# Optimization experiments

Hardware: AMD Instinct MI355X
Metric: run time of the kernel (lower is better)

The kernel has to match this reference:

```python
import jax, jax.numpy as jnp
import numpy as np

N_NODES = 100000
N_EDGES = 50000
NNZ = 800000
D_IN = 128
D_OUT = 128


def setup_inputs() -> dict:
    key = jax.random.key(0)
    k1, k2, k3, k4, k5 = jax.random.split(key, 5)
    x_0 = jax.random.normal(k1, (N_NODES, D_IN), dtype=jnp.float32)
    W = jax.random.normal(k2, (D_OUT, D_IN), dtype=jnp.float32) / np.sqrt(D_IN)
    b = jax.random.normal(k3, (D_OUT,), dtype=jnp.float32) * 0.01
    node_ids = jax.random.randint(k4, (NNZ,), 0, N_NODES, dtype=jnp.int32)
    edge_ids = jax.random.randint(k5, (NNZ,), 0, N_EDGES, dtype=jnp.int32)
    return {"x_0": x_0, "W": W, "b": b, "node_ids": node_ids, "edge_ids": edge_ids}


def reference(x_0, W, b, node_ids, edge_ids):
    # Linear transform (no batchnorm: use_bn=False)
    x = x_0 @ W.T + b  # [n_nodes, out_channels]

    # Step 1: hyperedge aggregation (e_aggr='sum'):  m_{0->1} = B_1^T x, reduce=sum
    m01 = jax.ops.segment_sum(x[node_ids], edge_ids, num_segments=N_EDGES)  # [n_edges, d]

    # Step 2: node aggregation (v_aggr='mean'):  m_{1->0} = B_1 m_{0->1}, reduce=mean
    s = jax.ops.segment_sum(m01[edge_ids], node_ids, num_segments=N_NODES)  # [n_nodes, d]
    cnt = jax.ops.segment_sum(jnp.ones((NNZ,), dtype=x.dtype), node_ids, num_segments=N_NODES)
    m10 = s / jnp.maximum(cnt, 1.0)[:, None]

    # Step 3: SAGE update (residual add)
    return x + m10
```

## Files before the change

kernel.cpp:

```cpp
#include <hip/hip_runtime.h>
#include <hip/hip_bf16.h>

#define NN 100000
#define NE 50000
#define NZ 800000
#define D  128
#define NSEG (NE + NN)
#define FILL_P 4
#define FILL_B 782
#define G_GEMM 782
#define G_HIST 391

typedef __bf16 bf16x8 __attribute__((ext_vector_type(8)));
typedef float f32x4 __attribute__((ext_vector_type(4)));

static __device__ __forceinline__ unsigned short f2bf(float f) {
  union { float f; unsigned u; } v; v.f = f;
  unsigned r = (v.u + 0x7FFFu + ((v.u >> 16) & 1u)) >> 16;
  return (unsigned short)r;
}
static __device__ __forceinline__ float bf2f(unsigned short h) {
  union { unsigned u; float f; } v; v.u = ((unsigned)h) << 16;
  return v.f;
}

__global__ __launch_bounds__(256) void unisage_gemm_hist(const float* __restrict__ x0,
                                                         const float* __restrict__ W,
                                                         const float* __restrict__ bias,
                                                         unsigned short* __restrict__ xb,
                                                         const int* __restrict__ nid,
                                                         const int* __restrict__ eid,
                                                         int* __restrict__ cnt,
                                                         unsigned short* __restrict__ rank_e,
                                                         unsigned short* __restrict__ rank_n) {
  __shared__ __bf16 Wl[128][136];
  if (blockIdx.x < G_HIST) {
    int base = (blockIdx.x * 256 + threadIdx.x) * 8;
    if (base >= NZ) return;
    int4 ea = *(const int4*)(eid + base);
    int4 eb = *(const int4*)(eid + base + 4);
    int4 na = *(const int4*)(nid + base);
    int4 nb = *(const int4*)(nid + base + 4);
    int e[8] = {ea.x, ea.y, ea.z, ea.w, eb.x, eb.y, eb.z, eb.w};
    int v[8] = {na.x, na.y, na.z, na.w, nb.x, nb.y, nb.z, nb.w};
    unsigned short re[8], rn[8];
#pragma unroll
    for (int j = 0; j < 8; ++j) re[j] = (unsigned short)atomicAdd(&cnt[e[j]], 1);
#pragma unroll
    for (int j = 0; j < 8; ++j) rn[j] = (unsigned short)atomicAdd(&cnt[NE + v[j]], 1);
    ushort4 r0 = {re[0], re[1], re[2], re[3]};
    ushort4 r1 = {re[4], re[5], re[6], re[7]};
    ushort4 s0 = {rn[0], rn[1], rn[2], rn[3]};
    ushort4 s1 = {rn[4], rn[5], rn[6], rn[7]};
    *(ushort4*)(rank_e + base) = r0;
    *(ushort4*)(rank_e + base + 4) = r1;
    *(ushort4*)(rank_n + base) = s0;
    *(ushort4*)(rank_n + base + 4) = s1;
  } else {
    const int t = threadIdx.x;
#pragma unroll
    for (int i = 0; i < 16; ++i) {
      int idx = i * 1024 + t * 4;
      int dout = idx >> 7;
      int k = idx & 127;
      float4 wv = *(const float4*)(W + idx);
      Wl[dout][k + 0] = (__bf16)wv.x;
      Wl[dout][k + 1] = (__bf16)wv.y;
      Wl[dout][k + 2] = (__bf16)wv.z;
      Wl[dout][k + 3] = (__bf16)wv.w;
    }
    __syncthreads();

    const int wave = t >> 6;
    const int lane = t & 63;
    const int lr = lane & 15;
    const int lg = lane >> 4;
    const int rowbase = (blockIdx.x - G_HIST) * 128 + wave * 32;

    f32x4 acc[2][8] = {};

#pragma unroll
    for (int ks = 0; ks < 4; ++ks) {
      const int k0 = ks * 32 + lg * 8;
      bf16x8 wf[8];
#pragma unroll
      for (int cf = 0; cf < 8; ++cf)
        wf[cf] = *(const bf16x8*)&Wl[cf * 16 + lr][k0];
#pragma unroll
      for (int rf = 0; rf < 2; ++rf) {
        int row = rowbase + rf * 16 + lr;
        row = row < NN ? row : NN - 1;
        const float* src = x0 + (size_t)row * D + k0;
        float4 f0 = *(const float4*)(src);
        float4 f1 = *(const float4*)(src + 4);
        bf16x8 xf;
        xf[0] = (__bf16)f0.x; xf[1] = (__bf16)f0.y;
        xf[2] = (__bf16)f0.z; xf[3] = (__bf16)f0.w;
        xf[4] = (__bf16)f1.x; xf[5] = (__bf16)f1.y;
        xf[6] = (__bf16)f1.z; xf[7] = (__bf16)f1.w;
#pragma unroll
        for (int cf = 0; cf < 8; ++cf)
          acc[rf][cf] = __builtin_amdgcn_mfma_f32_16x16x32_bf16(wf[cf], xf, acc[rf][cf], 0, 0, 0);
      }
    }

#pragma unroll
    for (int cf = 0; cf < 8; ++cf) {
      float4 bv = *(const float4*)(bias + cf * 16 + lg * 4);
#pragma unroll
      for (int rf = 0; rf < 2; ++rf) {
        int row = rowbase + rf * 16 + lr;
        if (row < NN) {
          ushort4 o;
          o.x = f2bf(acc[rf][cf][0] + bv.x);
          o.y = f2bf(acc[rf][cf][1] + bv.y);
          o.z = f2bf(acc[rf][cf][2] + bv.z);
          o.w = f2bf(acc[rf][cf][3] + bv.w);
          *(ushort4*)(xb + (size_t)row * D + cf * 16 + lg * 4) = o;
        }
      }
    }
  }
}

__global__ void unisage_scan_k1(const int* __restrict__ in, int* __restrict__ bsum, int n) {
  __shared__ int sh[256];
  int t = threadIdx.x;
  int base = blockIdx.x * 1024 + t * 4;
  int s = 0;
#pragma unroll
  for (int j = 0; j < 4; ++j)
    if (base + j < n) s += in[base + j];
  sh[t] = s;
  __syncthreads();
  for (int o = 128; o > 0; o >>= 1) {
    if (t < o) sh[t] += sh[t + o];
    __syncthreads();
  }
  if (t == 0) bsum[blockIdx.x] = sh[0];
}

__global__ void unisage_scan_k3(const int* __restrict__ in, const int* __restrict__ bsum,
                                int* __restrict__ out, int n, int nb) {
  __shared__ int sh[256];
  int t = threadIdx.x;
  int bv = (t < nb) ? bsum[t] : 0;
  sh[t] = bv;
  __syncthreads();
  for (int o = 1; o < 256; o <<= 1) {
    int add = (t >= o) ? sh[t - o] : 0;
    __syncthreads();
    sh[t] += add;
    __syncthreads();
  }
  int bbase = (blockIdx.x == 0) ? 0 : sh[blockIdx.x - 1];
  __syncthreads();

  int base = blockIdx.x * 1024 + t * 4;
  int v[4];
#pragma unroll
  for (int j = 0; j < 4; ++j) v[j] = (base + j < n) ? in[base + j] : 0;
  int tsum = v[0] + v[1] + v[2] + v[3];
  sh[t] = tsum;
  __syncthreads();
  for (int o = 1; o < 256; o <<= 1) {
    int add = (t >= o) ? sh[t - o] : 0;
    __syncthreads();
    sh[t] += add;
    __syncthreads();
  }
  int run = sh[t] - tsum + bbase;
#pragma unroll
  for (int j = 0; j < 4; ++j) {
    if (base + j < n) out[base + j] = run;
    run += v[j];
  }
}

__global__ void unisage_fill(const int* __restrict__ nid, const int* __restrict__ eid,
                             const unsigned short* __restrict__ rank_e,
                             const unsigned short* __restrict__ rank_n,
                             const int* __restrict__ off,
                             int* __restrict__ csr_e, int* __restrict__ csr_n) {
  const int R = (NSEG + FILL_P - 1) / FILL_P;
  int pass = blockIdx.x / FILL_B;
  int base = ((blockIdx.x % FILL_B) * 256 + threadIdx.x) * 4;
  if (base >= NZ) return;
  int lo = pass * R, hi = lo + R;
  int4 e4 = *(const int4*)(eid + base);
  int4 n4 = *(const int4*)(nid + base);
  ushort4 re4 = *(const ushort4*)(rank_e + base);
  ushort4 rn4 = *(const ushort4*)(rank_n + base);
  int e[4] = {e4.x, e4.y, e4.z, e4.w};
  int v[4] = {n4.x, n4.y, n4.z, n4.w};
  unsigned short re[4] = {re4.x, re4.y, re4.z, re4.w};
  unsigned short rn[4] = {rn4.x, rn4.y, rn4.z, rn4.w};
#pragma unroll
  for (int j = 0; j < 4; ++j) {
    if (e[j] >= lo && e[j] < hi) csr_e[off[e[j]] + (int)re[j]] = v[j];
    int s = NE + v[j];
    if (s >= lo && s < hi) csr_n[off[s] + (int)rn[j] - NZ] = e[j];
  }
}

#define QRED(x) { x += __shfl_xor(x, 16, 64); x += __shfl_xor(x, 32, 64); }

__global__ void unisage_edge_agg(const unsigned short* __restrict__ xb,
                                 const int* __restrict__ csr_e,
                                 const int* __restrict__ off, const int* __restrict__ cnt,
                                 unsigned short* __restrict__ m01b) {
  int w = (blockIdx.x * 256 + threadIdx.x) >> 6;
  int lane = threadIdx.x & 63;
  if (w >= NE) return;
  int quad = lane >> 4;
  int sl = lane & 15;
  int beg = off[w];
  int deg = cnt[w];
  int end = beg + deg;
  float a0 = 0, a1 = 0, a2 = 0, a3 = 0, a4 = 0, a5 = 0, a6 = 0, a7 = 0;
  for (int base = beg; base < end; base += 64) {
    int m = min(64, end - base);
    int idx = (lane < m) ? csr_e[base + lane] : 0;
    int iters = (m + 3) >> 2;
    for (int jj = 0; jj < iters; ++jj) {
      int p = 4 * jj + quad;
      int r = __shfl(idx, p, 64);
      if (p < m) {
        uint4 vv = *(const uint4*)(xb + (size_t)r * D + sl * 8);
        a0 += bf2f((unsigned short)(vv.x & 0xffffu)); a1 += bf2f((unsigned short)(vv.x >> 16));
        a2 += bf2f((unsigned short)(vv.y & 0xffffu)); a3 += bf2f((unsigned short)(vv.y >> 16));
        a4 += bf2f((unsigned short)(vv.z & 0xffffu)); a5 += bf2f((unsigned short)(vv.z >> 16));
        a6 += bf2f((unsigned short)(vv.w & 0xffffu)); a7 += bf2f((unsigned short)(vv.w >> 16));
      }
    }
  }
  QRED(a0) QRED(a1) QRED(a2) QRED(a3) QRED(a4) QRED(a5) QRED(a6) QRED(a7)
  if (quad == 0) {
    uint4 o;
    o.x = (unsigned)f2bf(a0) | ((unsigned)f2bf(a1) << 16);
    o.y = (unsigned)f2bf(a2) | ((unsigned)f2bf(a3) << 16);
    o.z = (unsigned)f2bf(a4) | ((unsigned)f2bf(a5) << 16);
    o.w = (unsigned)f2bf(a6) | ((unsigned)f2bf(a7) << 16);
    *(uint4*)(m01b + (size_t)w * D + sl * 8) = o;
  }
}

__global__ void unisage_node_agg(const unsigned short* __restrict__ xb,
                                 const unsigned short* __restrict__ m01b,
                                 const int* __restrict__ csr_n,
                                 const int* __restrict__ off, const int* __restrict__ cnt,
                                 float* __restrict__ out) {
  int wv = (blockIdx.x * 256 + threadIdx.x) >> 6;
  int lane = threadIdx.x & 63;
  int half = lane >> 5;
  int sub = lane & 31;
  int rg = sub >> 4;
  int sl = sub & 15;
  int w = wv * 2 + half;
  if (w >= NN) return;
  int deg = cnt[NE + w];
  int beg = off[NE + w] - NZ;
  int end = beg + deg;
  float a0 = 0, a1 = 0, a2 = 0, a3 = 0, a4 = 0, a5 = 0, a6 = 0, a7 = 0;
  for (int base = beg; base < end; base += 32) {
    int m = min(32, end - base);
    int idx = (sub < m) ? csr_n[base + sub] : 0;
    int iters = (m + 1) >> 1;
    for (int jj = 0; jj < iters; ++jj) {
      int p = 2 * jj + rg;
      int r = __shfl(idx, half * 32 + p, 64);
      if (p < m) {
        uint4 vv = *(const uint4*)(m01b + (size_t)r * D + sl * 8);
        a0 += bf2f((unsigned short)(vv.x & 0xffffu)); a1 += bf2f((unsigned short)(vv.x >> 16));
        a2 += bf2f((unsigned short)(vv.y & 0xffffu)); a3 += bf2f((unsigned short)(vv.y >> 16));
        a4 += bf2f((unsigned short)(vv.z & 0xffffu)); a5 += bf2f((unsigned short)(vv.z >> 16));
        a6 += bf2f((unsigned short)(vv.w & 0xffffu)); a7 += bf2f((unsigned short)(vv.w >> 16));
      }
    }
  }
  a0 += __shfl_xor(a0, 16, 64); a1 += __shfl_xor(a1, 16, 64);
  a2 += __shfl_xor(a2, 16, 64); a3 += __shfl_xor(a3, 16, 64);
  a4 += __shfl_xor(a4, 16, 64); a5 += __shfl_xor(a5, 16, 64);
  a6 += __shfl_xor(a6, 16, 64); a7 += __shfl_xor(a7, 16, 64);
  if (rg == 0) {
    float inv = 1.0f / fmaxf((float)deg, 1.0f);
    uint4 xr = *(const uint4*)(xb + (size_t)w * D + sl * 8);
    f32x4 o0, o1;
    o0[0] = bf2f((unsigned short)(xr.x & 0xffffu)) + a0 * inv;
    o0[1] = bf2f((unsigned short)(xr.x >> 16))     + a1 * inv;
    o0[2] = bf2f((unsigned short)(xr.y & 0xffffu)) + a2 * inv;
    o0[3] = bf2f((unsigned short)(xr.y >> 16))     + a3 * inv;
    o1[0] = bf2f((unsigned short)(xr.z & 0xffffu)) + a4 * inv;
    o1[1] = bf2f((unsigned short)(xr.z >> 16))     + a5 * inv;
    o1[2] = bf2f((unsigned short)(xr.w & 0xffffu)) + a6 * inv;
    o1[3] = bf2f((unsigned short)(xr.w >> 16))     + a7 * inv;
    __builtin_nontemporal_store(o0, (f32x4*)(out + (size_t)w * D + sl * 8));
    __builtin_nontemporal_store(o1, (f32x4*)(out + (size_t)w * D + sl * 8 + 4));
  }
}

extern "C" void kernel_launch(void* const* d_in, const int* in_sizes, int n_in,
                              void* d_out, int out_size, void* d_ws, size_t ws_size,
                              hipStream_t stream) {
  const float* x0   = (const float*)d_in[0];
  const float* W    = (const float*)d_in[1];
  const float* bias = (const float*)d_in[2];
  const int* nid    = (const int*)d_in[3];
  const int* eid    = (const int*)d_in[4];
  float* out = (float*)d_out;

  unsigned short* xb   = (unsigned short*)d_ws;
  unsigned short* m01b = xb + (size_t)NN * D;
  int* cnt   = (int*)(m01b + (size_t)NE * D);
  int* off   = cnt + 150016;
  unsigned short* rank_e = (unsigned short*)(off + 150016);
  unsigned short* rank_n = rank_e + NZ;
  int* csr_e = (int*)(rank_n + NZ);
  int* csr_n = csr_e + NZ;
  int* bsum  = csr_n + NZ;

  hipMemsetAsync(cnt, 0, NSEG * sizeof(int), stream);

  unisage_gemm_hist<<<G_HIST + G_GEMM, 256, 0, stream>>>(x0, W, bias, xb, nid, eid,
                                                         cnt, rank_e, rank_n);

  const int nb = (NSEG + 1023) / 1024;
  unisage_scan_k1<<<nb, 256, 0, stream>>>(cnt, bsum, NSEG);
  unisage_scan_k3<<<nb, 256, 0, stream>>>(cnt, bsum, off, NSEG, nb);

  unisage_fill<<<FILL_P * FILL_B, 256, 0, stream>>>(nid, eid, rank_e, rank_n, off, csr_e, csr_n);

  unisage_edge_agg<<<(NE * 64) / 256, 256, 0, stream>>>(xb, csr_e, off, cnt, m01b);
  unisage_node_agg<<<(NN / 2 * 64) / 256, 256, 0, stream>>>(xb, m01b, csr_n, off, cnt, out);
}
```

Baseline: 191.0 us.

## Split CSR fill and overlap node-side fill with edge aggregation

The combined fill kernel is split in two. The edge-CSR fill now runs alone in 2 passes over the edge range. The node-CSR fill, also 2 passes, is merged into the edge aggregation kernel as extra blocks, so those scatter writes run alongside the gather-sum instead of before it. This is meant to hide the node-side fill latency and drop its serialization. In exchange, the two block types in the merged launch now compete for bandwidth, and the edge fill is no longer split into the finer passes of the old 4-pass scheme.

New measurement: 189.0 us. No clear change (-1.1%).

```diff
diff --git a/kernel.cpp b/kernel.cpp
--- a/kernel.cpp
+++ b/kernel.cpp
@@ -6,10 +6,11 @@
 #define NZ 800000
 #define D  128
 #define NSEG (NE + NN)
-#define FILL_P 4
 #define FILL_B 782
 #define G_GEMM 782
 #define G_HIST 391
+#define G_EDGE 12500
+#define G_FILLN (2 * FILL_B)
 
 typedef __bf16 bf16x8 __attribute__((ext_vector_type(8)));
 typedef float f32x4 __attribute__((ext_vector_type(4)));
@@ -177,12 +178,11 @@
   }
 }
 
-__global__ void unisage_fill(const int* __restrict__ nid, const int* __restrict__ eid,
-                             const unsigned short* __restrict__ rank_e,
-                             const unsigned short* __restrict__ rank_n,
-                             const int* __restrict__ off,
-                             int* __restrict__ csr_e, int* __restrict__ csr_n) {
-  const int R = (NSEG + FILL_P - 1) / FILL_P;
+__global__ void unisage_fill_e(const int* __restrict__ nid, const int* __restrict__ eid,
+                               const unsigned short* __restrict__ rank_e,
+                               const int* __restrict__ off,
+                               int* __restrict__ csr_e) {
+  const int R = NE / 2;
   int pass = blockIdx.x / FILL_B;
   int base = ((blockIdx.x % FILL_B) * 256 + threadIdx.x) * 4;
   if (base >= NZ) return;
@@ -190,58 +190,76 @@
   int4 e4 = *(const int4*)(eid + base);
   int4 n4 = *(const int4*)(nid + base);
   ushort4 re4 = *(const ushort4*)(rank_e + base);
-  ushort4 rn4 = *(const ushort4*)(rank_n + base);
   int e[4] = {e4.x, e4.y, e4.z, e4.w};
   int v[4] = {n4.x, n4.y, n4.z, n4.w};
   unsigned short re[4] = {re4.x, re4.y, re4.z, re4.w};
-  unsigned short rn[4] = {rn4.x, rn4.y, rn4.z, rn4.w};
 #pragma unroll
   for (int j = 0; j < 4; ++j) {
     if (e[j] >= lo && e[j] < hi) csr_e[off[e[j]] + (int)re[j]] = v[j];
-    int s = NE + v[j];
-    if (s >= lo && s < hi) csr_n[off[s] + (int)rn[j] - NZ] = e[j];
   }
 }
 
 #define QRED(x) { x += __shfl_xor(x, 16, 64); x += __shfl_xor(x, 32, 64); }
 
-__global__ void unisage_edge_agg(const unsigned short* __restrict__ xb,
-                                 const int* __restrict__ csr_e,
-                                 const int* __restrict__ off, const int* __restrict__ cnt,
-                                 unsigned short* __restrict__ m01b) {
-  int w = (blockIdx.x * 256 + threadIdx.x) >> 6;
-  int lane = threadIdx.x & 63;
-  if (w >= NE) return;
-  int quad = lane >> 4;
-  int sl = lane & 15;
-  int beg = off[w];
-  int deg = cnt[w];
-  int end = beg + deg;
-  float a0 = 0, a1 = 0, a2 = 0, a3 = 0, a4 = 0, a5 = 0, a6 = 0, a7 = 0;
-  for (int base = beg; base < end; base += 64) {
-    int m = min(64, end - base);
-    int idx = (lane < m) ? csr_e[base + lane] : 0;
-    int iters = (m + 3) >> 2;
-    for (int jj = 0; jj < iters; ++jj) {
-      int p = 4 * jj + quad;
-      int r = __shfl(idx, p, 64);
-      if (p < m) {
-        uint4 vv = *(const uint4*)(xb + (size_t)r * D + sl * 8);
-        a0 += bf2f((unsigned short)(vv.x & 0xffffu)); a1 += bf2f((unsigned short)(vv.x >> 16));
-        a2 += bf2f((unsigned short)(vv.y & 0xffffu)); a3 += bf2f((unsigned short)(vv.y >> 16));
-        a4 += bf2f((unsigned short)(vv.z & 0xffffu)); a5 += bf2f((unsigned short)(vv.z >> 16));
-        a6 += bf2f((unsigned short)(vv.w & 0xffffu)); a7 += bf2f((unsigned short)(vv.w >> 16));
+__global__ void unisage_edge_fill(const unsigned short* __restrict__ xb,
+                                  const int* __restrict__ csr_e,
+                                  const int* __restrict__ off, const int* __restrict__ cnt,
+                                  unsigned short* __restrict__ m01b,
+                                  const int* __restrict__ nid, const int* __restrict__ eid,
+                                  const unsigned short* __restrict__ rank_n,
+                                  int* __restrict__ csr_n) {
+  if (blockIdx.x < G_FILLN) {
+    const int R = NN / 2;
+    int pass = blockIdx.x / FILL_B;
+    int base = ((blockIdx.x % FILL_B) * 256 + threadIdx.x) * 4;
+    if (base >= NZ) return;
+    int lo = NE + pass * R, hi = lo + R;
+    int4 e4 = *(const int4*)(eid + base);
+    int4 n4 = *(const int4*)(nid + base);
+    ushort4 rn4 = *(const ushort4*)(rank_n + base);
+    int e[4] = {e4.x, e4.y, e4.z, e4.w};
+    int v[4] = {n4.x, n4.y, n4.z, n4.w};
+    unsigned short rn[4] = {rn4.x, rn4.y, rn4.z, rn4.w};
+#pragma unroll
+    for (int j = 0; j < 4; ++j) {
+      int s = NE + v[j];
+      if (s >= lo && s < hi) csr_n[off[s] + (int)rn[j] - NZ] = e[j];
+    }
+  } else {
+    int w = ((blockIdx.x - G_FILLN) * 256 + threadIdx.x) >> 6;
+    int lane = threadIdx.x & 63;
+    if (w >= NE) return;
+    int quad = lane >> 4;
+    int sl = lane & 15;
+    int beg = off[w];
+    int deg = cnt[w];
+    int end = beg + deg;
+    float a0 = 0, a1 = 0, a2 = 0, a3 = 0, a4 = 0, a5 = 0, a6 = 0, a7 = 0;
+    for (int base = beg; base < end; base += 64) {
+      int m = min(64, end - base);
+      int idx = (lane < m) ? csr_e[base + lane] : 0;
+      int iters = (m + 3) >> 2;
+      for (int jj = 0; jj < iters; ++jj) {
+        int p = 4 * jj + quad;
+        int r = __shfl(idx, p, 64);
+        if (p < m) {
+          uint4 vv = *(const uint4*)(xb + (size_t)r * D + sl * 8);
+          a0 += bf2f((unsigned short)(vv.x & 0xffffu)); a1 += bf2f((unsigned short)(vv.x >> 16));
+          a2 += bf2f((unsigned short)(vv.y & 0xffffu)); a3 += bf2f((unsigned short)(vv.y >> 16));
+          a4 += bf2f((unsigned short)(vv.z & 0xffffu)); a5 += bf2f((unsigned short)(vv.z >> 16));
+          a6 += bf2f((unsigned short)(vv.w & 0xffffu)); a7 += bf2f((unsigned short)(vv.w >> 16));
+        }
       }
     }
-  }
-  QRED(a0) QRED(a1) QRED(a2) QRED(a3) QRED(a4) QRED(a5) QRED(a6) QRED(a7)
-  if (quad == 0) {
-    uint4 o;
-    o.x = (unsigned)f2bf(a0) | ((unsigned)f2bf(a1) << 16);
-    o.y = (unsigned)f2bf(a2) | ((unsigned)f2bf(a3) << 16);
-    o.z = (unsigned)f2bf(a4) | ((unsigned)f2bf(a5) << 16);
-    o.w = (unsigned)f2bf(a6) | ((unsigned)f2bf(a7) << 16);
-    *(uint4*)(m01b + (size_t)w * D + sl * 8) = o;
+    QRED(a0) QRED(a1) QRED(a2) QRED(a3) QRED(a4) QRED(a5) QRED(a6) QRED(a7)
+    if (quad == 0) {
+      uint4 o;
+      o.x = (unsigned)f2bf(a0) | ((unsigned)f2bf(a1) << 16);
+      o.y = (unsigned)f2bf(a2) | ((unsigned)f2bf(a3) << 16);
+      o.z = (unsigned)f2bf(a4) | ((unsigned)f2bf(a5) << 16);
+      o.w = (unsigned)f2bf(a6) | ((unsigned)f2bf(a7) << 16);
+      *(uint4*)(m01b + (size_t)w * D + sl * 8) = o;
+    }
   }
 }
 
@@ -328,8 +346,10 @@
   unisage_scan_k1<<<nb, 256, 0, stream>>>(cnt, bsum, NSEG);
   unisage_scan_k3<<<nb, 256, 0, stream>>>(cnt, bsum, off, NSEG, nb);
 
-  unisage_fill<<<FILL_P * FILL_B, 256, 0, stream>>>(nid, eid, rank_e, rank_n, off, csr_e, csr_n);
-
-  unisage_edge_agg<<<(NE * 64) / 256, 256, 0, stream>>>(xb, csr_e, off, cnt, m01b);
+  unisage_fill_e<<<2 * FILL_B, 256, 0, stream>>>(nid, eid, rank_e, off, csr_e);
+
+  unisage_edge_fill<<<G_FILLN + G_EDGE, 256, 0, stream>>>(xb, csr_e, off, cnt, m01b,
+                                                          nid, eid, rank_n, csr_n);
+
   unisage_node_agg<<<(NN / 2 * 64) / 256, 256, 0, stream>>>(xb, m01b, csr_n, off, cnt, out);
 }
```
